# Performance work log

Hardware: AMD Instinct MI355X
Metric: run time of the kernel (lower is better)

## Reference

```python
import jax, jax.numpy as jnp
import numpy as np

MI, DIS, DIN, HID, L, H, NG, H1, OUT = 2048, 1024, 3072, 256, 15, 8, 8, 512, 64
DENOM = 4.0 / 7.0  # (grid_max - grid_min) / (num_grids - 1)
EPS = 1e-5


def _ln(x, g, b):
    m = jnp.mean(x, axis=-1, keepdims=True)
    v = jnp.mean((x - m) ** 2, axis=-1, keepdims=True)
    return (x - m) * jax.lax.rsqrt(v + EPS) * g + b


def _fastkan(x, ln_g, ln_b, grid, Ws, Wb, bb):
    xn = _ln(x, ln_g, ln_b)
    basis = jnp.exp(-(((xn[..., None] - grid) / DENOM) ** 2))  # [N, DIN, NG]
    ret = basis.reshape(x.shape[0], -1) @ Ws.T                  # SplineLinear (no bias)
    return ret + jax.nn.silu(x) @ Wb.T + bb                      # base update


def _hgcn(x, G, W, attn, bias, rW1, rb1, rW2, rb2, ln_g, ln_b, jk_W, jk_b):
    # per-layer multi-head conv: mean_h a_h * G @ (x @ W_h) == G @ (x @ (sum_h a_h W_h / H))
    def step(xc, p):
        W_l, a_l, b_l, rW1_l, rb1_l, rW2_l, rb2_l, g_l, be_l = p
        W_eff = jnp.einsum('h,hio->io', a_l, W_l) / H
        out = G @ (xc @ W_eff) + b_l
        gate = jax.nn.sigmoid(jax.nn.relu(out @ rW1_l.T + rb1_l) @ rW2_l.T + rb2_l)
        out = _ln(out * gate, g_l, be_l)
        out = jnp.where(out >= 0, out, 0.25 * out)  # leaky_relu(0.25); dropout off (eval)
        return out, out
    _, outs = jax.lax.scan(step, x, (W, attn, bias, rW1, rb1, rW2, rb2, ln_g, ln_b))
    jk = jnp.moveaxis(outs, 0, 1).reshape(x.shape[0], L * HID)   # jumping-knowledge concat
    return jk @ jk_W.T + jk_b


def _mlp3(x, W1, b1, W2, b2, W3, b3):
    h = jax.nn.relu(x @ W1.T + b1)
    h = jax.nn.relu(h @ W2.T + b2)
    return jax.nn.relu(h @ W3.T + b3)


def _forward(concat_mi, concat_dis, G_mi, G_dis, AT, A, rbf_grid, mi_kan_ln_g, mi_kan_ln_b, mi_kan_Ws, mi_kan_Wb, mi_kan_bb, dis_kan_ln_g, dis_kan_ln_b, dis_kan_Ws, dis_kan_Wb, dis_kan_bb, mi_W, mi_attn, mi_bias, mi_rW1, mi_rb1, mi_rW2, mi_rb2, mi_ln_g, mi_ln_b, mi_jk_W, mi_jk_b, dis_W, dis_attn, dis_bias, dis_rW1, dis_rb1, dis_rW2, dis_rb2, dis_ln_g, dis_ln_b, dis_jk_W, dis_jk_b, lx_W1, lx_b1, lx_W2, lx_b2, lx_W3, lx_b3, ly_W1, ly_b1, ly_W2, ly_b2, ly_W3, ly_b3, ne_W, ne_b, he_W, he_b, mun_W, mun_b, mue_W, mue_b):
    # AT and A are accepted by the original forward but never used in its body.
    mi_e = _fastkan(concat_mi, mi_kan_ln_g, mi_kan_ln_b, rbf_grid, mi_kan_Ws, mi_kan_Wb, mi_kan_bb)
    dis_e = _fastkan(concat_dis, dis_kan_ln_g, dis_kan_ln_b, rbf_grid, dis_kan_Ws, dis_kan_Wb, dis_kan_bb)
    mi_f = _hgcn(mi_e, G_mi, mi_W, mi_attn, mi_bias, mi_rW1, mi_rb1, mi_rW2, mi_rb2, mi_ln_g, mi_ln_b, mi_jk_W, mi_jk_b)
    dis_f = _hgcn(dis_e, G_dis, dis_W, dis_attn, dis_bias, dis_rW1, dis_rb1, dis_rW2, dis_rb2, dis_ln_g, dis_ln_b, dis_jk_W, dis_jk_b)
    x = _mlp3(mi_f, lx_W1, lx_b1, lx_W2, lx_b2, lx_W3, lx_b3)
    y = _mlp3(dis_f, ly_W1, ly_b1, ly_W2, ly_b2, ly_W3, ly_b3)
    result_h = x @ y.T                                           # [MI, DIS]
    z_node = jax.nn.relu(concat_mi @ ne_W.T + ne_b)              # node_encoders1 (eval: no dropout)
    z_edge = jax.nn.relu(concat_dis @ he_W.T + he_b)             # hyperedge_encoders1
    z_node_mean = z_node @ mun_W.T + mun_b                       # _enc_mu_node (identity act)
    z_edge_mean = z_edge @ mue_W.T + mue_b                       # _enc_mu_hedge
    recon = z_node_mean @ z_edge_mean.T                          # decoder2 with identity act
    score = 0.7 * jax.nn.sigmoid(recon) + 0.3 * jax.nn.sigmoid(result_h)
    return score, recon


def setup_inputs() -> dict:
    ks = iter(jax.random.split(jax.random.key(0), 96))
    nrm = lambda shape, s: jax.random.normal(next(ks), shape, dtype=jnp.float32) * s
    uni = lambda shape: jax.random.uniform(next(ks), shape, dtype=jnp.float32)
    d = {}
    d['concat_mi'] = nrm((MI, DIN), 1.0)
    d['concat_dis'] = nrm((DIS, DIN), 1.0)
    d['G_mi'] = uni((MI, MI)) / MI    # row-normalized dense hypergraph adjacency
    d['G_dis'] = uni((DIS, DIS)) / DIS
    d['AT'] = uni((DIS, MI))
    d['A'] = uni((MI, DIS))
    d['rbf_grid'] = jnp.linspace(-2.0, 2.0, NG).astype(jnp.float32)
    for p in ('mi', 'dis'):
        d[p + '_kan_ln_g'] = jnp.ones((DIN,), jnp.float32)
        d[p + '_kan_ln_b'] = jnp.zeros((DIN,), jnp.float32)
        d[p + '_kan_Ws'] = nrm((HID, DIN * NG), 0.02)
        d[p + '_kan_Wb'] = nrm((HID, DIN), 0.02)
        d[p + '_kan_bb'] = nrm((HID,), 0.01)
        d[p + '_W'] = nrm((L, H, HID, HID), 0.06)
        d[p + '_attn'] = jnp.ones((L, H), jnp.float32)
        d[p + '_bias'] = nrm((L, HID), 0.01)
        d[p + '_rW1'] = nrm((L, HID // 4, HID), 0.05)
        d[p + '_rb1'] = nrm((L, HID // 4), 0.01)
        d[p + '_rW2'] = nrm((L, HID, HID // 4), 0.05)
        d[p + '_rb2'] = nrm((L, HID), 0.01)
        d[p + '_ln_g'] = jnp.ones((L, HID), jnp.float32)
        d[p + '_ln_b'] = jnp.zeros((L, HID), jnp.float32)
        d[p + '_jk_W'] = nrm((HID, L * HID), 0.02)
        d[p + '_jk_b'] = nrm((HID,), 0.01)
    for p in ('lx', 'ly'):
        d[p + '_W1'] = nrm((256, HID), 0.05); d[p + '_b1'] = nrm((256,), 0.01)
        d[p + '_W2'] = nrm((128, 256), 0.05); d[p + '_b2'] = nrm((128,), 0.01)
        d[p + '_W3'] = nrm((64, 128), 0.05); d[p + '_b3'] = nrm((64,), 0.01)
    d['ne_W'] = nrm((H1, DIN), 0.02); d['ne_b'] = nrm((H1,), 0.01)
    d['he_W'] = nrm((H1, DIN), 0.02); d['he_b'] = nrm((H1,), 0.01)
    d['mun_W'] = nrm((OUT, H1), 0.02); d['mun_b'] = nrm((OUT,), 0.01)
    d['mue_W'] = nrm((OUT, H1), 0.02); d['mue_b'] = nrm((OUT,), 0.01)
    return d


def reference(concat_mi, concat_dis, G_mi, G_dis, AT, A, rbf_grid, mi_kan_ln_g, mi_kan_ln_b, mi_kan_Ws, mi_kan_Wb, mi_kan_bb, dis_kan_ln_g, dis_kan_ln_b, dis_kan_Ws, dis_kan_Wb, dis_kan_bb, mi_W, mi_attn, mi_bias, mi_rW1, mi_rb1, mi_rW2, mi_rb2, mi_ln_g, mi_ln_b, mi_jk_W, mi_jk_b, dis_W, dis_attn, dis_bias, dis_rW1, dis_rb1, dis_rW2, dis_rb2, dis_ln_g, dis_ln_b, dis_jk_W, dis_jk_b, lx_W1, lx_b1, lx_W2, lx_b2, lx_W3, lx_b3, ly_W1, ly_b1, ly_W2, ly_b2, ly_W3, ly_b3, ne_W, ne_b, he_W, he_b, mun_W, mun_b, mue_W, mue_b):
    return _forward(concat_mi, concat_dis, G_mi, G_dis, AT, A, rbf_grid, mi_kan_ln_g, mi_kan_ln_b, mi_kan_Ws, mi_kan_Wb, mi_kan_bb, dis_kan_ln_g, dis_kan_ln_b, dis_kan_Ws, dis_kan_Wb, dis_kan_bb, mi_W, mi_attn, mi_bias, mi_rW1, mi_rb1, mi_rW2, mi_rb2, mi_ln_g, mi_ln_b, mi_jk_W, mi_jk_b, dis_W, dis_attn, dis_bias, dis_rW1, dis_rb1, dis_rW2, dis_rb2, dis_ln_g, dis_ln_b, dis_jk_W, dis_jk_b, lx_W1, lx_b1, lx_W2, lx_b2, lx_W3, lx_b3, ly_W1, ly_b1, ly_W2, ly_b2, ly_W3, ly_b3, ne_W, ne_b, he_W, he_b, mun_W, mun_b, mue_W, mue_b)
```

## Files before the change

### kernel.cpp

```cpp
#include <hip/hip_runtime.h>
#include <cstdint>
#include <cstddef>

typedef unsigned short u16;
typedef __attribute__((ext_vector_type(8))) short short8;
typedef __attribute__((ext_vector_type(4))) float f32x4;

#define MI_N  2048
#define DIS_N 1024
#define TOT_N 3072
#define DIN   3072
#define HID   256
#define LL    15
#define NG    8

__device__ __forceinline__ float b2f(u16 u) {
  unsigned int v = ((unsigned int)u) << 16;
  float f;
  __builtin_memcpy(&f, &v, 4);
  return f;
}
__device__ __forceinline__ u16 f2b(float f) {
  unsigned int u;
  __builtin_memcpy(&u, &f, 4);
  u = (u + 0x7fffu + ((u >> 16) & 1u)) >> 16;
  return (u16)u;
}
__device__ __forceinline__ float sigf(float x) { return 1.f / (1.f + __expf(-x)); }

#define NSEG 20
struct CvtJobs {
  const float* src[NSEG];
  u16* dst[NSEG];
  int nblk[NSEG];
  int nseg;
};

__global__ __launch_bounds__(256) void cvt_f2b(CvtJobs j) {
  int b = blockIdx.x, s = 0;
  while (s + 1 < j.nseg && b >= j.nblk[s]) { b -= j.nblk[s]; ++s; }
  const long base = ((long)b * 256 + threadIdx.x) * 8;
  const float4 v0 = *(const float4*)(j.src[s] + base);
  const float4 v1 = *(const float4*)(j.src[s] + base + 4);
  short8 o;
  o[0] = (short)f2b(v0.x); o[1] = (short)f2b(v0.y);
  o[2] = (short)f2b(v0.z); o[3] = (short)f2b(v0.w);
  o[4] = (short)f2b(v1.x); o[5] = (short)f2b(v1.y);
  o[6] = (short)f2b(v1.z); o[7] = (short)f2b(v1.w);
  *(short8*)(j.dst[s] + base) = o;
}

struct GP {
  const u16* A; int lda;
  const u16* B; int ldb;
  void* C; int ldc;
  const float* bias;
  int K;
  int mblk;
};

template <int ACT, int TRANS, int F32OUT, int NCT>
__global__ __launch_bounds__(256) void gemm_bt(GP p0, GP p1) {
  GP p = p0;
  int bx = blockIdx.x;
  if (bx >= p0.mblk) { bx -= p0.mblk; p = p1; }
  const int tid = threadIdx.x;
  const int w = tid >> 6;
  const int lane = tid & 63;
  const int m16 = lane & 15, quad = lane >> 4;
  const int kph = quad * 8;
  const long row0 = (long)bx * 32 + m16;
  const long colBase = (long)blockIdx.y * (16 * NCT);
  f32x4 acc[2][NCT] = {};
  const u16* A0 = p.A + row0 * (long)p.lda + kph;
  const u16* A1 = A0 + 16L * p.lda;
  const u16* Bb = p.B + (colBase + m16) * (long)p.ldb + kph;
  const long bstep = 16L * p.ldb;
  for (int kk = w * 32; kk < p.K; kk += 128) {
    short8 a0 = *(const short8*)(A0 + kk);
    short8 a1 = *(const short8*)(A1 + kk);
#pragma unroll
    for (int c = 0; c < NCT; ++c) {
      short8 b = *(const short8*)(Bb + c * bstep + kk);
      acc[0][c] = __builtin_amdgcn_mfma_f32_16x16x32_bf16(a0, b, acc[0][c], 0, 0, 0);
      acc[1][c] = __builtin_amdgcn_mfma_f32_16x16x32_bf16(a1, b, acc[1][c], 0, 0, 0);
    }
  }
  __shared__ float red[2][64][NCT * 8 + 1];
  float* av = (float*)acc;
  if (w >= 2) {
#pragma unroll
    for (int i = 0; i < NCT * 8; ++i) red[w - 2][lane][i] = av[i];
  }
  __syncthreads();
  if (w < 2) {
#pragma unroll
    for (int i = 0; i < NCT * 8; ++i) av[i] += red[w][lane][i];
  }
  __syncthreads();
  if (w == 1) {
#pragma unroll
    for (int i = 0; i < NCT * 8; ++i) red[0][lane][i] = av[i];
  }
  __syncthreads();
  if (w != 0) return;
#pragma unroll
  for (int i = 0; i < NCT * 8; ++i) av[i] += red[0][lane][i];
#pragma unroll
  for (int c = 0; c < NCT; ++c) {
    const long col = colBase + c * 16 + m16;
    const float bv = p.bias ? p.bias[col] : 0.f;
#pragma unroll
    for (int r = 0; r < 2; ++r) {
      const long orow = (long)bx * 32 + r * 16 + quad * 4;
#pragma unroll
      for (int j = 0; j < 4; ++j) {
        float v = acc[r][c][j] + bv;
        if (ACT == 1) v = fmaxf(v, 0.f);
        if (ACT == 2) v = sigf(v);
        if (F32OUT)
          ((float*)p.C)[(orow + j) * (long)p.ldc + col] = v;
        else if (TRANS)
          ((u16*)p.C)[col * (long)p.ldc + orow + j] = f2b(v);
        else
          ((u16*)p.C)[(orow + j) * (long)p.ldc + col] = f2b(v);
      }
    }
  }
}

struct FKP {
  const u16* xn; const u16* xb;
  const u16* Ws; const u16* Wb;
  float* partial;
  int rowoff;
  int mblk;
};

__global__ __launch_bounds__(256) void fastkan_gemm(FKP p0, FKP p1, const float* grid8) {
  FKP p = p0;
  int bx = blockIdx.x;
  if (bx >= p0.mblk) { bx -= p0.mblk; p = p1; }
  const int chunk = blockIdx.z;
  const int tid = threadIdx.x;
  const int w = tid >> 6;
  const int lane = tid & 63;
  const int m16 = lane & 15, quad = lane >> 4, kph = quad * 8;
  const long row0 = (long)bx * 32 + m16;
  const long colBase = (long)blockIdx.y * 128;
  f32x4 acc[2][8] = {};
  if (chunk < 4) {
    float gv[8];
#pragma unroll
    for (int j = 0; j < 8; ++j) gv[j] = grid8[j];
    const u16* xn0 = p.xn + row0 * (long)DIN;
    const u16* xn1 = xn0 + 16L * DIN;
    const int k0 = chunk * 6144, k1 = k0 + 6144;
    for (int kk = k0 + w * 32; kk < k1; kk += 128) {
      const int d = (kk >> 3) + quad;
      const float x0 = b2f(xn0[d]);
      const float x1 = b2f(xn1[d]);
      short8 a0, a1;
#pragma unroll
      for (int j = 0; j < 8; ++j) {
        float t0 = (x0 - gv[j]) * 1.75f;
        float t1 = (x1 - gv[j]) * 1.75f;
        a0[j] = (short)f2b(__expf(-t0 * t0));
        a1[j] = (short)f2b(__expf(-t1 * t1));
      }
#pragma unroll
      for (int c = 0; c < 8; ++c) {
        const u16* Bp = p.Ws + (colBase + c * 16 + m16) * (long)(DIN * NG) + kk + kph;
        short8 b = *(const short8*)Bp;
        acc[0][c] = __builtin_amdgcn_mfma_f32_16x16x32_bf16(a0, b, acc[0][c], 0, 0, 0);
        acc[1][c] = __builtin_amdgcn_mfma_f32_16x16x32_bf16(a1, b, acc[1][c], 0, 0, 0);
      }
    }
  } else {
    const u16* x0p = p.xb + row0 * (long)DIN + kph;
    const u16* x1p = x0p + 16L * DIN;
    for (int kk = w * 32; kk < DIN; kk += 128) {
      short8 r0 = *(const short8*)(x0p + kk);
      short8 r1 = *(const short8*)(x1p + kk);
      short8 a0, a1;
#pragma unroll
      for (int j = 0; j < 8; ++j) {
        float v0 = b2f((u16)r0[j]);
        float v1 = b2f((u16)r1[j]);
        a0[j] = (short)f2b(v0 * sigf(v0));
        a1[j] = (short)f2b(v1 * sigf(v1));
      }
#pragma unroll
      for (int c = 0; c < 8; ++c) {
        const u16* Bp = p.Wb + (colBase + c * 16 + m16) * (long)DIN + kk + kph;
        short8 b = *(const short8*)Bp;
        acc[0][c] = __builtin_amdgcn_mfma_f32_16x16x32_bf16(a0, b, acc[0][c], 0, 0, 0);
        acc[1][c] = __builtin_amdgcn_mfma_f32_16x16x32_bf16(a1, b, acc[1][c], 0, 0, 0);
      }
    }
  }
  __shared__ float red[2][64][65];
  float* av = (float*)acc;
  if (w >= 2) {
#pragma unroll
    for (int i = 0; i < 64; ++i) red[w - 2][lane][i] = av[i];
  }
  __syncthreads();
  if (w < 2) {
#pragma unroll
    for (int i = 0; i < 64; ++i) av[i] += red[w][lane][i];
  }
  __syncthreads();
  if (w == 1) {
#pragma unroll
    for (int i = 0; i < 64; ++i) red[0][lane][i] = av[i];
  }
  __syncthreads();
  if (w != 0) return;
#pragma unroll
  for (int i = 0; i < 64; ++i) av[i] += red[0][lane][i];
  float* outp = p.partial + ((long)chunk * TOT_N + p.rowoff) * HID;
#pragma unroll
  for (int c = 0; c < 8; ++c) {
    const long col = colBase + c * 16 + m16;
#pragma unroll
    for (int r = 0; r < 2; ++r) {
      const long orow = (long)bx * 32 + r * 16 + quad * 4;
#pragma unroll
      for (int j = 0; j < 4; ++j) outp[(orow + j) * HID + col] = acc[r][c][j];
    }
  }
}

__global__ __launch_bounds__(256) void fk_combine(const float* partial, const float* bb_mi,
                                                  const float* bb_dis, u16* e) {
  const long i = (long)blockIdx.x * 256 + threadIdx.x;
  const int c = (int)(i & 255);
  const long n = i >> 8;
  float s = 0.f;
#pragma unroll
  for (int pI = 0; pI < 5; ++pI) s += partial[(long)pI * TOT_N * HID + i];
  s += (n < MI_N ? bb_mi : bb_dis)[c];
  e[i] = f2b(s);
}

__global__ __launch_bounds__(256) void weff_kernel(const float* Wmi, const float* Ami,
                                                   const float* Wdis, const float* Adis,
                                                   u16* outT) {
  const int b = blockIdx.x;
  const int s = b / 3840;
  const int r = b % 3840;
  const int l = r >> 8;
  const int t = r & 255;
  const int i0 = (t >> 4) << 4;
  const int o0 = (t & 15) << 4;
  const float* W = (s ? Wdis : Wmi) + (long)l * 8 * 65536;
  const float* A = (s ? Adis : Ami) + l * 8;
  const int tx = threadIdx.x & 15;
  const int ty = threadIdx.x >> 4;
  float sum = 0.f;
#pragma unroll
  for (int h = 0; h < 8; ++h)
    sum += A[h] * W[(long)h * 65536 + (long)(i0 + ty) * 256 + o0 + tx];
  sum *= 0.125f;
  __shared__ float tile[16][17];
  tile[ty][tx] = sum;
  __syncthreads();
  outT[((long)s * LL + l) * 65536 + (long)(o0 + ty) * 256 + i0 + tx] = f2b(tile[tx][ty]);
}

__device__ __forceinline__ void breduce2(float& a, float& b) {
  for (int o = 32; o > 0; o >>= 1) {
    a += __shfl_down(a, o);
    b += __shfl_down(b, o);
  }
  __shared__ float sm[8];
  const int w = threadIdx.x >> 6;
  const int lane = threadIdx.x & 63;
  if (lane == 0) { sm[w] = a; sm[4 + w] = b; }
  __syncthreads();
  if (threadIdx.x == 0) {
    sm[0] = sm[0] + sm[1] + sm[2] + sm[3];
    sm[4] = sm[4] + sm[5] + sm[6] + sm[7];
  }
  __syncthreads();
  a = sm[0];
  b = sm[4];
}

__global__ __launch_bounds__(256) void ln_silu(const float* xmi, const float* xdis,
                                               const float* gmi, const float* bmi,
                                               const float* gdis, const float* bdis,
                                               u16* xn, u16* cbf) {
  const int n = blockIdx.x;
  const bool ds = (n >= MI_N);
  const float* x = ds ? xdis + (long)(n - MI_N) * DIN : xmi + (long)n * DIN;
  const float* g = ds ? gdis : gmi;
  const float* be = ds ? bdis : bmi;
  float xv[12];
  float s1 = 0.f, s2 = 0.f;
#pragma unroll
  for (int j = 0; j < 12; ++j) {
    xv[j] = x[j * 256 + threadIdx.x];
    s1 += xv[j];
    s2 += xv[j] * xv[j];
  }
  breduce2(s1, s2);
  const float m = s1 * (1.f / DIN);
  const float inv = rsqrtf(s2 * (1.f / DIN) - m * m + 1e-5f);
#pragma unroll
  for (int j = 0; j < 12; ++j) {
    const int e = j * 256 + threadIdx.x;
    xn[(long)n * DIN + e] = f2b((xv[j] - m) * inv * g[e] + be[e]);
    cbf[(long)n * DIN + e] = f2b(xv[j]);
  }
}

__global__ __launch_bounds__(256) void gate_ln(const u16* hout, const u16* gate,
                                               const float* gmi, const float* bmi,
                                               const float* gdis, const float* bdis,
                                               u16* jk, int l) {
  const int n = blockIdx.x;
  const int c = threadIdx.x;
  const bool ds = (n >= MI_N);
  const float* g = (ds ? gdis : gmi) + l * HID;
  const float* be = (ds ? bdis : bmi) + l * HID;
  const float h = b2f(hout[(long)n * HID + c]) * b2f(gate[(long)n * HID + c]);
  float s1 = h, s2 = h * h;
  breduce2(s1, s2);
  const float m = s1 * (1.f / HID);
  const float var = s2 * (1.f / HID) - m * m;
  float y = (h - m) * rsqrtf(var + 1e-5f) * g[c] + be[c];
  y = (y >= 0.f) ? y : 0.25f * y;
  jk[(long)n * (LL * HID) + l * HID + c] = f2b(y);
}

__global__ __launch_bounds__(256) void final_combine(const float* rh, float* out) {
  const long i = (long)blockIdx.x * 256 + threadIdx.x;
  const float rc = out[(long)MI_N * DIS_N + i];
  out[i] = 0.7f * sigf(rc) + 0.3f * sigf(rh[i]);
}

extern "C" void kernel_launch(void* const* d_in, const int* in_sizes, int n_in,
                              void* d_out, int out_size, void* d_ws, size_t ws_size,
                              hipStream_t stream) {
  const float* concat_mi   = (const float*)d_in[0];
  const float* concat_dis  = (const float*)d_in[1];
  const float* G_mi        = (const float*)d_in[2];
  const float* G_dis       = (const float*)d_in[3];
  const float* rbf_grid    = (const float*)d_in[6];
  const float* mi_kan_ln_g = (const float*)d_in[7];
  const float* mi_kan_ln_b = (const float*)d_in[8];
  const float* mi_kan_Ws   = (const float*)d_in[9];
  const float* mi_kan_Wb   = (const float*)d_in[10];
  const float* mi_kan_bb   = (const float*)d_in[11];
  const float* mi_W        = (const float*)d_in[12];
  const float* mi_attn     = (const float*)d_in[13];
  const float* mi_bias     = (const float*)d_in[14];
  const float* mi_rW1      = (const float*)d_in[15];
  const float* mi_rb1      = (const float*)d_in[16];
  const float* mi_rW2      = (const float*)d_in[17];
  const float* mi_rb2      = (const float*)d_in[18];
  const float* mi_ln_g     = (const float*)d_in[19];
  const float* mi_ln_b     = (const float*)d_in[20];
  const float* mi_jk_W     = (const float*)d_in[21];
  const float* mi_jk_b     = (const float*)d_in[22];
  const float* dis_kan_ln_g = (const float*)d_in[23];
  const float* dis_kan_ln_b = (const float*)d_in[24];
  const float* dis_kan_Ws  = (const float*)d_in[25];
  const float* dis_kan_Wb  = (const float*)d_in[26];
  const float* dis_kan_bb  = (const float*)d_in[27];
  const float* dis_W       = (const float*)d_in[28];
  const float* dis_attn    = (const float*)d_in[29];
  const float* dis_bias    = (const float*)d_in[30];
  const float* dis_rW1     = (const float*)d_in[31];
  const float* dis_rb1     = (const float*)d_in[32];
  const float* dis_rW2     = (const float*)d_in[33];
  const float* dis_rb2     = (const float*)d_in[34];
  const float* dis_ln_g    = (const float*)d_in[35];
  const float* dis_ln_b    = (const float*)d_in[36];
  const float* dis_jk_W    = (const float*)d_in[37];
  const float* dis_jk_b    = (const float*)d_in[38];
  const float* lx_W1 = (const float*)d_in[39]; const float* lx_b1 = (const float*)d_in[40];
  const float* lx_W2 = (const float*)d_in[41]; const float* lx_b2 = (const float*)d_in[42];
  const float* lx_W3 = (const float*)d_in[43]; const float* lx_b3 = (const float*)d_in[44];
  const float* ly_W1 = (const float*)d_in[45]; const float* ly_b1 = (const float*)d_in[46];
  const float* ly_W2 = (const float*)d_in[47]; const float* ly_b2 = (const float*)d_in[48];
  const float* ly_W3 = (const float*)d_in[49]; const float* ly_b3 = (const float*)d_in[50];
  const float* ne_W  = (const float*)d_in[51]; const float* ne_b  = (const float*)d_in[52];
  const float* he_W  = (const float*)d_in[53]; const float* he_b  = (const float*)d_in[54];
  const float* mun_W = (const float*)d_in[55]; const float* mun_b = (const float*)d_in[56];
  const float* mue_W = (const float*)d_in[57]; const float* mue_b = (const float*)d_in[58];

  char* wp = (char*)d_ws;
  size_t off = 0;
  auto alloc = [&](size_t bytes) -> void* {
    void* p = wp + off;
    off += (bytes + 255) & ~(size_t)255;
    return p;
  };
  u16* cbf    = (u16*)alloc((size_t)TOT_N * DIN * 2);
  u16* gmib   = (u16*)alloc((size_t)MI_N * MI_N * 2);
  u16* gdisb  = (u16*)alloc((size_t)DIS_N * DIS_N * 2);
  u16* wsb0   = (u16*)alloc((size_t)256 * 24576 * 2);
  u16* wsb1   = (u16*)alloc((size_t)256 * 24576 * 2);
  u16* wbb0   = (u16*)alloc((size_t)256 * 3072 * 2);
  u16* wbb1   = (u16*)alloc((size_t)256 * 3072 * 2);
  u16* jkwb0  = (u16*)alloc((size_t)256 * 3840 * 2);
  u16* jkwb1  = (u16*)alloc((size_t)256 * 3840 * 2);
  u16* rw1b0  = (u16*)alloc((size_t)LL * 64 * 256 * 2);
  u16* rw1b1  = (u16*)alloc((size_t)LL * 64 * 256 * 2);
  u16* rw2b0  = (u16*)alloc((size_t)LL * 256 * 64 * 2);
  u16* rw2b1  = (u16*)alloc((size_t)LL * 256 * 64 * 2);
  u16* lxw1b  = (u16*)alloc((size_t)256 * 256 * 2);
  u16* lxw2b  = (u16*)alloc((size_t)128 * 256 * 2);
  u16* lxw3b  = (u16*)alloc((size_t)64 * 128 * 2);
  u16* lyw1b  = (u16*)alloc((size_t)256 * 256 * 2);
  u16* lyw2b  = (u16*)alloc((size_t)128 * 256 * 2);
  u16* lyw3b  = (u16*)alloc((size_t)64 * 128 * 2);
  u16* neb    = (u16*)alloc((size_t)512 * 3072 * 2);
  u16* heb    = (u16*)alloc((size_t)512 * 3072 * 2);
  u16* munb   = (u16*)alloc((size_t)64 * 512 * 2);
  u16* mueb   = (u16*)alloc((size_t)64 * 512 * 2);
  u16* wefft  = (u16*)alloc((size_t)2 * LL * 65536 * 2);
  u16* e      = (u16*)alloc((size_t)TOT_N * HID * 2);
  u16* t1t    = (u16*)alloc((size_t)HID * TOT_N * 2);
  u16* hout   = (u16*)alloc((size_t)TOT_N * HID * 2);
  u16* g1b    = (u16*)alloc((size_t)TOT_N * 64 * 2);
  u16* gateb  = (u16*)alloc((size_t)TOT_N * HID * 2);
  u16* jk     = (u16*)alloc((size_t)TOT_N * LL * HID * 2);
  u16* fb     = (u16*)alloc((size_t)TOT_N * HID * 2);
  char* regA  = (char*)alloc(35000000);
  u16* xn     = (u16*)regA;
  float* fkp  = (float*)(regA + 18874624);
  u16* h1b    = (u16*)regA;
  u16* h2b    = (u16*)(regA + 1572864);
  u16* xyb    = (u16*)(regA + 2359296);
  float* rh   = (float*)(regA + 2752512);
  u16* zb     = (u16*)(regA + 11141120);
  u16* zm     = (u16*)(regA + 14286848);
  float* outf = (float*)d_out;
  float* rec  = outf + (size_t)MI_N * DIS_N;
  (void)ws_size; (void)in_sizes; (void)n_in; (void)out_size;

  const dim3 B256(256);

  {
    CvtJobs cj{};
    int ns = 0, total = 0;
    auto push = [&](const float* s, u16* dst, int count) {
      cj.src[ns] = s; cj.dst[ns] = dst; cj.nblk[ns] = count / 2048;
      total += count / 2048; ++ns;
    };
    push(G_mi, gmib, MI_N * MI_N);
    push(G_dis, gdisb, DIS_N * DIS_N);
    push(mi_kan_Ws, wsb0, 256 * 24576);
    push(dis_kan_Ws, wsb1, 256 * 24576);
    push(mi_kan_Wb, wbb0, 256 * 3072);
    push(dis_kan_Wb, wbb1, 256 * 3072);
    push(mi_jk_W, jkwb0, 256 * 3840);
    push(dis_jk_W, jkwb1, 256 * 3840);
    push(mi_rW1, rw1b0, LL * 64 * 256);
    push(dis_rW1, rw1b1, LL * 64 * 256);
    push(mi_rW2, rw2b0, LL * 256 * 64);
    push(dis_rW2, rw2b1, LL * 256 * 64);
    push(lx_W1, lxw1b, 256 * 256);
    push(lx_W2, lxw2b, 128 * 256);
    push(lx_W3, lxw3b, 64 * 128);
    push(ly_W1, lyw1b, 256 * 256);
    push(ly_W2, lyw2b, 128 * 256);
    push(ly_W3, lyw3b, 64 * 128);
    push(ne_W, neb, 512 * 3072);
    push(he_W, heb, 512 * 3072);
    cj.nseg = ns;
    cvt_f2b<<<dim3(total), B256, 0, stream>>>(cj);
    CvtJobs cj2{};
    cj2.src[0] = mun_W; cj2.dst[0] = munb; cj2.nblk[0] = (64 * 512) / 2048;
    cj2.src[1] = mue_W; cj2.dst[1] = mueb; cj2.nblk[1] = (64 * 512) / 2048;
    cj2.nseg = 2;
    cvt_f2b<<<dim3(32), B256, 0, stream>>>(cj2);
  }
  ln_silu<<<dim3(TOT_N), B256, 0, stream>>>(concat_mi, concat_dis, mi_kan_ln_g, mi_kan_ln_b,
                                            dis_kan_ln_g, dis_kan_ln_b, xn, cbf);
  weff_kernel<<<dim3(2 * LL * 256), B256, 0, stream>>>(mi_W, mi_attn, dis_W, dis_attn, wefft);
  {
    FKP f0{xn, cbf, wsb0, wbb0, fkp, 0, 64};
    FKP f1{xn + (size_t)MI_N * DIN, cbf + (size_t)MI_N * DIN, wsb1, wbb1, fkp, MI_N, 32};
    fastkan_gemm<<<dim3(96, 2, 5), B256, 0, stream>>>(f0, f1, rbf_grid);
    fk_combine<<<dim3(TOT_N * HID / 256), B256, 0, stream>>>(fkp, mi_kan_bb, dis_kan_bb, e);
  }
  for (int l = 0; l < LL; ++l) {
    const u16* xc0 = (l == 0) ? e : jk + (size_t)(l - 1) * HID;
    const u16* xc1 = (l == 0) ? e + (size_t)MI_N * HID
                              : jk + (size_t)MI_N * LL * HID + (size_t)(l - 1) * HID;
    const int xlda = (l == 0) ? HID : LL * HID;
    GP a0{xc0, xlda, wefft + (size_t)l * 65536, 256, t1t, MI_N, nullptr, 256, 64};
    GP a1{xc1, xlda, wefft + ((size_t)LL + l) * 65536, 256, t1t + (size_t)HID * MI_N, DIS_N,
          nullptr, 256, 32};
    gemm_bt<0, 1, 0, 4><<<dim3(96, 4), B256, 0, stream>>>(a0, a1);
    GP h0{gmib, MI_N, t1t, MI_N, hout, HID, mi_bias + l * HID, MI_N, 64};
    GP h1{gdisb, DIS_N, t1t + (size_t)HID * MI_N, DIS_N, hout + (size_t)MI_N * HID, HID,
          dis_bias + l * HID, DIS_N, 32};
    gemm_bt<0, 0, 0, 4><<<dim3(96, 4), B256, 0, stream>>>(h0, h1);
    GP g0{hout, HID, rw1b0 + (size_t)l * 64 * HID, HID, g1b, 64, mi_rb1 + l * 64, HID, 64};
    GP g1{hout + (size_t)MI_N * HID, HID, rw1b1 + (size_t)l * 64 * HID, HID,
          g1b + (size_t)MI_N * 64, 64, dis_rb1 + l * 64, HID, 32};
    gemm_bt<1, 0, 0, 4><<<dim3(96, 1), B256, 0, stream>>>(g0, g1);
    GP s0{g1b, 64, rw2b0 + (size_t)l * HID * 64, 64, gateb, HID, mi_rb2 + l * HID, 64, 64};
    GP s1{g1b + (size_t)MI_N * 64, 64, rw2b1 + (size_t)l * HID * 64, 64,
          gateb + (size_t)MI_N * HID, HID, dis_rb2 + l * HID, 64, 32};
    gemm_bt<2, 0, 0, 4><<<dim3(96, 4), B256, 0, stream>>>(s0, s1);
    gate_ln<<<dim3(TOT_N), B256, 0, stream>>>(hout, gateb, mi_ln_g, mi_ln_b, dis_ln_g,
                                              dis_ln_b, jk, l);
  }
  {
    GP j0{jk, LL * HID, jkwb0, LL * HID, fb, HID, mi_jk_b, LL * HID, 64};
    GP j1{jk + (size_t)MI_N * LL * HID, LL * HID, jkwb1, LL * HID, fb + (size_t)MI_N * HID,
          HID, dis_jk_b, LL * HID, 32};
    gemm_bt<0, 0, 0, 4><<<dim3(96, 4), B256, 0, stream>>>(j0, j1);
  }
  {
    GP m0{fb, HID, lxw1b, HID, h1b, 256, lx_b1, HID, 64};
    GP m1{fb + (size_t)MI_N * HID, HID, lyw1b, HID, h1b + (size_t)MI_N * 256, 256, ly_b1,
          HID, 32};
    gemm_bt<1, 0, 0, 4><<<dim3(96, 4), B256, 0, stream>>>(m0, m1);
    GP n0{h1b, 256, lxw2b, 256, h2b, 128, lx_b2, 256, 64};
    GP n1{h1b + (size_t)MI_N * 256, 256, lyw2b, 256, h2b + (size_t)MI_N * 128, 128, ly_b2,
          256, 32};
    gemm_bt<1, 0, 0, 4><<<dim3(96, 2), B256, 0, stream>>>(n0, n1);
    GP o0{h2b, 128, lxw3b, 128, xyb, 64, lx_b3, 128, 64};
    GP o1{h2b + (size_t)MI_N * 128, 128, lyw3b, 128, xyb + (size_t)MI_N * 64, 64, ly_b3,
          128, 32};
    gemm_bt<1, 0, 0, 4><<<dim3(96, 1), B256, 0, stream>>>(o0, o1);
  }
  {
    GP r0{xyb, 64, xyb + (size_t)MI_N * 64, 64, rh, DIS_N, nullptr, 64, 64};
    gemm_bt<0, 0, 1, 4><<<dim3(64, 16), B256, 0, stream>>>(r0, r0);
  }
  {
    GP e0{cbf, DIN, neb, DIN, zb, 512, ne_b, DIN, 64};
    GP e1{cbf + (size_t)MI_N * DIN, DIN, heb, DIN, zb + (size_t)MI_N * 512, 512, he_b, DIN,
          32};
    gemm_bt<1, 0, 0, 4><<<dim3(96, 8), B256, 0, stream>>>(e0, e1);
  }
  {
    GP u0{zb, 512, munb, 512, zm, 64, mun_b, 512, 64};
    GP u1{zb + (size_t)MI_N * 512, 512, mueb, 512, zm + (size_t)MI_N * 64, 64, mue_b, 512,
          32};
    gemm_bt<0, 0, 0, 4><<<dim3(96, 1), B256, 0, stream>>>(u0, u1);
  }
  {
    GP c0{zm, 64, zm + (size_t)MI_N * 64, 64, rec, DIS_N, nullptr, 64, 64};
    gemm_bt<0, 0, 1, 4><<<dim3(64, 16), B256, 0, stream>>>(c0, c0);
  }
  final_combine<<<dim3(MI_N * DIS_N / 256), B256, 0, stream>>>(rh, outf);
}
```

Baseline: 1.458 ms.

## Retile FastKAN GEMM to full-width 16-row tiles with deeper split-K

The FastKAN spline/base GEMM now gives each block 16 rows and all 256 output columns, instead of 32 rows by 128 columns. Split-K grows from 5 to 9 chunks, and the combine kernel and partial buffer are enlarged to match. Each Gaussian RBF basis value is now computed once per row rather than once per column block, and per-thread x values are prefetched into registers. Pairs of floats are packed to bf16 with v_cvt_pk_bf16_f32. The trade-off is that each weight load now feeds one MFMA instead of two, so weight traffic through L2 roughly doubles, and the larger split-K means more partial-sum writes and reads.

```diff
diff --git a/kernel.cpp b/kernel.cpp
--- a/kernel.cpp
+++ b/kernel.cpp
@@ -27,6 +27,11 @@
   return (u16)u;
 }
 __device__ __forceinline__ float sigf(float x) { return 1.f / (1.f + __expf(-x)); }
+__device__ __forceinline__ unsigned cvtpk(float a, float b) {
+  unsigned r;
+  asm("v_cvt_pk_bf16_f32 %0, %1, %2" : "=v"(r) : "v"(a), "v"(b));
+  return r;
+}
 
 #define NSEG 20
 struct CvtJobs {
@@ -146,56 +151,52 @@
   const int w = tid >> 6;
   const int lane = tid & 63;
   const int m16 = lane & 15, quad = lane >> 4, kph = quad * 8;
-  const long row0 = (long)bx * 32 + m16;
-  const long colBase = (long)blockIdx.y * 128;
-  f32x4 acc[2][8] = {};
-  if (chunk < 4) {
+  const long row0 = (long)bx * 16 + m16;
+  f32x4 acc[16] = {};
+  if (chunk < 8) {
     float gv[8];
 #pragma unroll
     for (int j = 0; j < 8; ++j) gv[j] = grid8[j];
     const u16* xn0 = p.xn + row0 * (long)DIN;
-    const u16* xn1 = xn0 + 16L * DIN;
-    const int k0 = chunk * 6144, k1 = k0 + 6144;
-    for (int kk = k0 + w * 32; kk < k1; kk += 128) {
-      const int d = (kk >> 3) + quad;
-      const float x0 = b2f(xn0[d]);
-      const float x1 = b2f(xn1[d]);
-      short8 a0, a1;
-#pragma unroll
-      for (int j = 0; j < 8; ++j) {
-        float t0 = (x0 - gv[j]) * 1.75f;
-        float t1 = (x1 - gv[j]) * 1.75f;
-        a0[j] = (short)f2b(__expf(-t0 * t0));
-        a1[j] = (short)f2b(__expf(-t1 * t1));
+    const int d0 = chunk * 384 + w * 4 + quad;
+    u16 xr[24];
+#pragma unroll
+    for (int t = 0; t < 24; ++t) xr[t] = xn0[d0 + 16 * t];
+    const u16* Bb = p.Ws + (long)m16 * (DIN * NG) + chunk * 3072 + w * 32 + kph;
+#pragma unroll 2
+    for (int t = 0; t < 24; ++t) {
+      const float x0 = b2f(xr[t]);
+      union { short8 s; unsigned u[4]; } a0;
+#pragma unroll
+      for (int jj = 0; jj < 4; ++jj) {
+        float da = x0 - gv[2 * jj];
+        float db = x0 - gv[2 * jj + 1];
+        a0.u[jj] = cvtpk(__expf(da * da * -3.0625f), __expf(db * db * -3.0625f));
       }
 #pragma unroll
-      for (int c = 0; c < 8; ++c) {
-        const u16* Bp = p.Ws + (colBase + c * 16 + m16) * (long)(DIN * NG) + kk + kph;
-        short8 b = *(const short8*)Bp;
-        acc[0][c] = __builtin_amdgcn_mfma_f32_16x16x32_bf16(a0, b, acc[0][c], 0, 0, 0);
-        acc[1][c] = __builtin_amdgcn_mfma_f32_16x16x32_bf16(a1, b, acc[1][c], 0, 0, 0);
+      for (int c = 0; c < 16; ++c) {
+        short8 b = *(const short8*)(Bb + (long)c * (16 * DIN * NG) + t * 128);
+        acc[c] = __builtin_amdgcn_mfma_f32_16x16x32_bf16(a0.s, b, acc[c], 0, 0, 0);
       }
     }
   } else {
     const u16* x0p = p.xb + row0 * (long)DIN + kph;
-    const u16* x1p = x0p + 16L * DIN;
-    for (int kk = w * 32; kk < DIN; kk += 128) {
+    const u16* Bb = p.Wb + (long)m16 * DIN + w * 32 + kph;
+#pragma unroll 2
+    for (int t = 0; t < 24; ++t) {
+      const int kk = w * 32 + t * 128;
       short8 r0 = *(const short8*)(x0p + kk);
-      short8 r1 = *(const short8*)(x1p + kk);
-      short8 a0, a1;
-#pragma unroll
-      for (int j = 0; j < 8; ++j) {
-        float v0 = b2f((u16)r0[j]);
-        float v1 = b2f((u16)r1[j]);
-        a0[j] = (short)f2b(v0 * sigf(v0));
-        a1[j] = (short)f2b(v1 * sigf(v1));
+      union { short8 s; unsigned u[4]; } a0;
+#pragma unroll
+      for (int jj = 0; jj < 4; ++jj) {
+        float va = b2f((u16)r0[2 * jj]);
+        float vb = b2f((u16)r0[2 * jj + 1]);
+        a0.u[jj] = cvtpk(va * sigf(va), vb * sigf(vb));
       }
 #pragma unroll
-      for (int c = 0; c < 8; ++c) {
-        const u16* Bp = p.Wb + (colBase + c * 16 + m16) * (long)DIN + kk + kph;
-        short8 b = *(const short8*)Bp;
-        acc[0][c] = __builtin_amdgcn_mfma_f32_16x16x32_bf16(a0, b, acc[0][c], 0, 0, 0);
-        acc[1][c] = __builtin_amdgcn_mfma_f32_16x16x32_bf16(a1, b, acc[1][c], 0, 0, 0);
+      for (int c = 0; c < 16; ++c) {
+        short8 b = *(const short8*)(Bb + (long)c * (16 * DIN) + t * 128);
+        acc[c] = __builtin_amdgcn_mfma_f32_16x16x32_bf16(a0.s, b, acc[c], 0, 0, 0);
       }
     }
   }
@@ -221,14 +222,11 @@
   for (int i = 0; i < 64; ++i) av[i] += red[0][lane][i];
   float* outp = p.partial + ((long)chunk * TOT_N + p.rowoff) * HID;
 #pragma unroll
-  for (int c = 0; c < 8; ++c) {
-    const long col = colBase + c * 16 + m16;
-#pragma unroll
-    for (int r = 0; r < 2; ++r) {
-      const long orow = (long)bx * 32 + r * 16 + quad * 4;
-#pragma unroll
-      for (int j = 0; j < 4; ++j) outp[(orow + j) * HID + col] = acc[r][c][j];
-    }
+  for (int c = 0; c < 16; ++c) {
+    const long col = c * 16 + m16;
+    const long orow = (long)bx * 16 + quad * 4;
+#pragma unroll
+    for (int j = 0; j < 4; ++j) outp[(orow + j) * HID + col] = acc[c][j];
   }
 }
 
@@ -239,7 +237,7 @@
   const long n = i >> 8;
   float s = 0.f;
 #pragma unroll
-  for (int pI = 0; pI < 5; ++pI) s += partial[(long)pI * TOT_N * HID + i];
+  for (int pI = 0; pI < 9; ++pI) s += partial[(long)pI * TOT_N * HID + i];
   s += (n < MI_N ? bb_mi : bb_dis)[c];
   e[i] = f2b(s);
 }
@@ -430,7 +428,7 @@
   u16* gateb  = (u16*)alloc((size_t)TOT_N * HID * 2);
   u16* jk     = (u16*)alloc((size_t)TOT_N * LL * HID * 2);
   u16* fb     = (u16*)alloc((size_t)TOT_N * HID * 2);
-  char* regA  = (char*)alloc(35000000);
+  char* regA  = (char*)alloc(47300000);
   u16* xn     = (u16*)regA;
   float* fkp  = (float*)(regA + 18874624);
   u16* h1b    = (u16*)regA;
@@ -484,9 +482,9 @@
                                             dis_kan_ln_g, dis_kan_ln_b, xn, cbf);
   weff_kernel<<<dim3(2 * LL * 256), B256, 0, stream>>>(mi_W, mi_attn, dis_W, dis_attn, wefft);
   {
-    FKP f0{xn, cbf, wsb0, wbb0, fkp, 0, 64};
-    FKP f1{xn + (size_t)MI_N * DIN, cbf + (size_t)MI_N * DIN, wsb1, wbb1, fkp, MI_N, 32};
-    fastkan_gemm<<<dim3(96, 2, 5), B256, 0, stream>>>(f0, f1, rbf_grid);
+    FKP f0{xn, cbf, wsb0, wbb0, fkp, 0, 128};
+    FKP f1{xn + (size_t)MI_N * DIN, cbf + (size_t)MI_N * DIN, wsb1, wbb1, fkp, MI_N, 64};
+    fastkan_gemm<<<dim3(192, 1, 9), B256, 0, stream>>>(f0, f1, rbf_grid);
     fk_combine<<<dim3(TOT_N * HID / 256), B256, 0, stream>>>(fkp, mi_kan_bb, dis_kan_bb, e);
   }
   for (int l = 0; l < LL; ++l) {
```

Result: slower. 1.601 ms (+9.8%).

## Fuse per-layer HGCN chain into one kernel with next-layer projection

Applied to the files above, without the earlier changes.

Each layer's propagation GEMM, both gate GEMMs, the sigmoid gate, the layernorm with leaky ReLU, and the next layer's x@W_eff projection now run in a single kernel. Intermediates stay in shared memory, and the transposed projection is ping-ponged between two buffers. This cuts five launches per layer down to one and removes the global round trips for hout, g1 and the gate. In exchange only 96 blocks run, each with a full-K G-row GEMM that has no LDS staging of operands, so parallelism and memory efficiency per layer may drop.

```diff
diff --git a/kernel.cpp b/kernel.cpp
--- a/kernel.cpp
+++ b/kernel.cpp
@@ -244,6 +244,159 @@
   e[i] = f2b(s);
 }
 
+struct HLP {
+  const u16* G; const u16* t1t; u16* t1t_next; const u16* weff_next;
+  const float* bias; const u16* rw1; const float* rb1;
+  const u16* rw2; const float* rb2; const float* lng; const float* lnb;
+  u16* jk; int M; int mblk;
+};
+
+__global__ __launch_bounds__(256) void hgcn_layer(HLP p0, HLP p1) {
+  HLP p = p0;
+  int bx = blockIdx.x;
+  if (bx >= p0.mblk) { bx -= p0.mblk; p = p1; }
+  const int tid = threadIdx.x;
+  const int w = tid >> 6, lane = tid & 63;
+  const int m16 = lane & 15, quad = lane >> 4, kph = quad * 8;
+  const int cb = w * 64;
+  const long row0 = (long)bx * 32;
+  __shared__ __align__(16) u16 hl[32][264];
+  __shared__ __align__(16) u16 gl[32][264];
+  __shared__ __align__(16) u16 g1l[32][72];
+
+  {
+    f32x4 acc[2][4] = {};
+    const u16* A0 = p.G + (row0 + m16) * (long)p.M + kph;
+    const u16* A1 = A0 + 16L * p.M;
+    const u16* Bb = p.t1t + (long)(cb + m16) * p.M + kph;
+    const long bstep = 16L * p.M;
+    for (int kk = 0; kk < p.M; kk += 32) {
+      short8 a0 = *(const short8*)(A0 + kk);
+      short8 a1 = *(const short8*)(A1 + kk);
+#pragma unroll
+      for (int c = 0; c < 4; ++c) {
+        short8 b = *(const short8*)(Bb + c * bstep + kk);
+        acc[0][c] = __builtin_amdgcn_mfma_f32_16x16x32_bf16(a0, b, acc[0][c], 0, 0, 0);
+        acc[1][c] = __builtin_amdgcn_mfma_f32_16x16x32_bf16(a1, b, acc[1][c], 0, 0, 0);
+      }
+    }
+#pragma unroll
+    for (int c = 0; c < 4; ++c) {
+      const int col = cb + c * 16 + m16;
+      const float bv = p.bias[col];
+#pragma unroll
+      for (int r = 0; r < 2; ++r) {
+        const int orow = r * 16 + quad * 4;
+#pragma unroll
+        for (int j = 0; j < 4; ++j) hl[orow + j][col] = f2b(acc[r][c][j] + bv);
+      }
+    }
+  }
+  __syncthreads();
+  {
+    f32x4 acc[2] = {};
+    const u16* Bb = p.rw1 + (long)(w * 16 + m16) * 256 + kph;
+#pragma unroll
+    for (int kk = 0; kk < 256; kk += 32) {
+      short8 a0 = *(const short8*)&hl[m16][kk + kph];
+      short8 a1 = *(const short8*)&hl[16 + m16][kk + kph];
+      short8 b = *(const short8*)(Bb + kk);
+      acc[0] = __builtin_amdgcn_mfma_f32_16x16x32_bf16(a0, b, acc[0], 0, 0, 0);
+      acc[1] = __builtin_amdgcn_mfma_f32_16x16x32_bf16(a1, b, acc[1], 0, 0, 0);
+    }
+    const int col = w * 16 + m16;
+    const float bv = p.rb1[col];
+#pragma unroll
+    for (int r = 0; r < 2; ++r) {
+      const int orow = r * 16 + quad * 4;
+#pragma unroll
+      for (int j = 0; j < 4; ++j) g1l[orow + j][col] = f2b(fmaxf(acc[r][j] + bv, 0.f));
+    }
+  }
+  __syncthreads();
+  {
+    f32x4 acc[2][4] = {};
+    const u16* Bb = p.rw2 + (long)(cb + m16) * 64 + kph;
+#pragma unroll
+    for (int kk = 0; kk < 64; kk += 32) {
+      short8 a0 = *(const short8*)&g1l[m16][kk + kph];
+      short8 a1 = *(const short8*)&g1l[16 + m16][kk + kph];
+#pragma unroll
+      for (int c = 0; c < 4; ++c) {
+        short8 b = *(const short8*)(Bb + c * (16L * 64) + kk);
+        acc[0][c] = __builtin_amdgcn_mfma_f32_16x16x32_bf16(a0, b, acc[0][c], 0, 0, 0);
+        acc[1][c] = __builtin_amdgcn_mfma_f32_16x16x32_bf16(a1, b, acc[1][c], 0, 0, 0);
+      }
+    }
+#pragma unroll
+    for (int c = 0; c < 4; ++c) {
+      const int col = cb + c * 16 + m16;
+      const float bv = p.rb2[col];
+#pragma unroll
+      for (int r = 0; r < 2; ++r) {
+        const int orow = r * 16 + quad * 4;
+#pragma unroll
+        for (int j = 0; j < 4; ++j) gl[orow + j][col] = f2b(sigf(acc[r][c][j] + bv));
+      }
+    }
+  }
+  __syncthreads();
+  {
+    const int row = tid >> 3;
+    const int sub = tid & 7;
+    float pv[32];
+    float s1 = 0.f, s2 = 0.f;
+#pragma unroll
+    for (int i = 0; i < 32; ++i) {
+      const int col = sub * 32 + i;
+      const float v = b2f(hl[row][col]) * b2f(gl[row][col]);
+      pv[i] = v; s1 += v; s2 += v * v;
+    }
+#pragma unroll
+    for (int o = 1; o < 8; o <<= 1) { s1 += __shfl_xor(s1, o); s2 += __shfl_xor(s2, o); }
+    const float m = s1 * (1.f / HID);
+    const float inv = rsqrtf(s2 * (1.f / HID) - m * m + 1e-5f);
+    u16* jrow = p.jk + (row0 + row) * (long)(LL * HID);
+#pragma unroll
+    for (int i = 0; i < 32; ++i) {
+      const int col = sub * 32 + i;
+      float y = (pv[i] - m) * inv * p.lng[col] + p.lnb[col];
+      y = (y >= 0.f) ? y : 0.25f * y;
+      const u16 yb = f2b(y);
+      jrow[col] = yb;
+      gl[row][col] = yb;
+    }
+  }
+  if (!p.weff_next) return;
+  __syncthreads();
+  {
+    f32x4 acc[2][4] = {};
+    const u16* Bb = p.weff_next + (long)(cb + m16) * 256 + kph;
+#pragma unroll
+    for (int kk = 0; kk < 256; kk += 32) {
+      short8 a0 = *(const short8*)&gl[m16][kk + kph];
+      short8 a1 = *(const short8*)&gl[16 + m16][kk + kph];
+#pragma unroll
+      for (int c = 0; c < 4; ++c) {
+        short8 b = *(const short8*)(Bb + c * (16L * 256) + kk);
+        acc[0][c] = __builtin_amdgcn_mfma_f32_16x16x32_bf16(a0, b, acc[0][c], 0, 0, 0);
+        acc[1][c] = __builtin_amdgcn_mfma_f32_16x16x32_bf16(a1, b, acc[1][c], 0, 0, 0);
+      }
+    }
+#pragma unroll
+    for (int c = 0; c < 4; ++c) {
+      const long col = cb + c * 16 + m16;
+#pragma unroll
+      for (int r = 0; r < 2; ++r) {
+        const int orow = r * 16 + quad * 4;
+#pragma unroll
+        for (int j = 0; j < 4; ++j)
+          p.t1t_next[col * (long)p.M + row0 + orow + j] = f2b(acc[r][c][j]);
+      }
+    }
+  }
+}
+
 __global__ __launch_bounds__(256) void weff_kernel(const float* Wmi, const float* Ami,
                                                    const float* Wdis, const float* Adis,
                                                    u16* outT) {
@@ -314,25 +467,6 @@
     xn[(long)n * DIN + e] = f2b((xv[j] - m) * inv * g[e] + be[e]);
     cbf[(long)n * DIN + e] = f2b(xv[j]);
   }
-}
-
-__global__ __launch_bounds__(256) void gate_ln(const u16* hout, const u16* gate,
-                                               const float* gmi, const float* bmi,
-                                               const float* gdis, const float* bdis,
-                                               u16* jk, int l) {
-  const int n = blockIdx.x;
-  const int c = threadIdx.x;
-  const bool ds = (n >= MI_N);
-  const float* g = (ds ? gdis : gmi) + l * HID;
-  const float* be = (ds ? bdis : bmi) + l * HID;
-  const float h = b2f(hout[(long)n * HID + c]) * b2f(gate[(long)n * HID + c]);
-  float s1 = h, s2 = h * h;
-  breduce2(s1, s2);
-  const float m = s1 * (1.f / HID);
-  const float var = s2 * (1.f / HID) - m * m;
-  float y = (h - m) * rsqrtf(var + 1e-5f) * g[c] + be[c];
-  y = (y >= 0.f) ? y : 0.25f * y;
-  jk[(long)n * (LL * HID) + l * HID + c] = f2b(y);
 }
 
 __global__ __launch_bounds__(256) void final_combine(const float* rh, float* out) {
@@ -425,9 +559,7 @@
   u16* wefft  = (u16*)alloc((size_t)2 * LL * 65536 * 2);
   u16* e      = (u16*)alloc((size_t)TOT_N * HID * 2);
   u16* t1t    = (u16*)alloc((size_t)HID * TOT_N * 2);
-  u16* hout   = (u16*)alloc((size_t)TOT_N * HID * 2);
-  u16* g1b    = (u16*)alloc((size_t)TOT_N * 64 * 2);
-  u16* gateb  = (u16*)alloc((size_t)TOT_N * HID * 2);
+  u16* t1t2   = (u16*)alloc((size_t)HID * TOT_N * 2);
   u16* jk     = (u16*)alloc((size_t)TOT_N * LL * HID * 2);
   u16* fb     = (u16*)alloc((size_t)TOT_N * HID * 2);
   char* regA  = (char*)alloc(35000000);
@@ -489,29 +621,30 @@
     fastkan_gemm<<<dim3(96, 2, 5), B256, 0, stream>>>(f0, f1, rbf_grid);
     fk_combine<<<dim3(TOT_N * HID / 256), B256, 0, stream>>>(fkp, mi_kan_bb, dis_kan_bb, e);
   }
-  for (int l = 0; l < LL; ++l) {
-    const u16* xc0 = (l == 0) ? e : jk + (size_t)(l - 1) * HID;
-    const u16* xc1 = (l == 0) ? e + (size_t)MI_N * HID
-                              : jk + (size_t)MI_N * LL * HID + (size_t)(l - 1) * HID;
-    const int xlda = (l == 0) ? HID : LL * HID;
-    GP a0{xc0, xlda, wefft + (size_t)l * 65536, 256, t1t, MI_N, nullptr, 256, 64};
-    GP a1{xc1, xlda, wefft + ((size_t)LL + l) * 65536, 256, t1t + (size_t)HID * MI_N, DIS_N,
-          nullptr, 256, 32};
+  {
+    GP a0{e, HID, wefft, 256, t1t, MI_N, nullptr, 256, 64};
+    GP a1{e + (size_t)MI_N * HID, HID, wefft + (size_t)LL * 65536, 256,
+          t1t + (size_t)HID * MI_N, DIS_N, nullptr, 256, 32};
     gemm_bt<0, 1, 0, 4><<<dim3(96, 4), B256, 0, stream>>>(a0, a1);
-    GP h0{gmib, MI_N, t1t, MI_N, hout, HID, mi_bias + l * HID, MI_N, 64};
-    GP h1{gdisb, DIS_N, t1t + (size_t)HID * MI_N, DIS_N, hout + (size_t)MI_N * HID, HID,
-          dis_bias + l * HID, DIS_N, 32};
-    gemm_bt<0, 0, 0, 4><<<dim3(96, 4), B256, 0, stream>>>(h0, h1);
-    GP g0{hout, HID, rw1b0 + (size_t)l * 64 * HID, HID, g1b, 64, mi_rb1 + l * 64, HID, 64};
-    GP g1{hout + (size_t)MI_N * HID, HID, rw1b1 + (size_t)l * 64 * HID, HID,
-          g1b + (size_t)MI_N * 64, 64, dis_rb1 + l * 64, HID, 32};
-    gemm_bt<1, 0, 0, 4><<<dim3(96, 1), B256, 0, stream>>>(g0, g1);
-    GP s0{g1b, 64, rw2b0 + (size_t)l * HID * 64, 64, gateb, HID, mi_rb2 + l * HID, 64, 64};
-    GP s1{g1b + (size_t)MI_N * 64, 64, rw2b1 + (size_t)l * HID * 64, 64,
-          gateb + (size_t)MI_N * HID, HID, dis_rb2 + l * HID, 64, 32};
-    gemm_bt<2, 0, 0, 4><<<dim3(96, 4), B256, 0, stream>>>(s0, s1);
-    gate_ln<<<dim3(TOT_N), B256, 0, stream>>>(hout, gateb, mi_ln_g, mi_ln_b, dis_ln_g,
-                                              dis_ln_b, jk, l);
+  }
+  {
+    u16* tc = t1t;
+    u16* tn = t1t2;
+    for (int l = 0; l < LL; ++l) {
+      const bool last = (l == LL - 1);
+      HLP h0{gmib, tc, tn, last ? nullptr : wefft + (size_t)(l + 1) * 65536,
+             mi_bias + l * HID, rw1b0 + (size_t)l * 64 * HID, mi_rb1 + l * 64,
+             rw2b0 + (size_t)l * HID * 64, mi_rb2 + l * HID,
+             mi_ln_g + l * HID, mi_ln_b + l * HID, jk + (size_t)l * HID, MI_N, 64};
+      HLP h1{gdisb, tc + (size_t)HID * MI_N, tn + (size_t)HID * MI_N,
+             last ? nullptr : wefft + ((size_t)LL + l + 1) * 65536,
+             dis_bias + l * HID, rw1b1 + (size_t)l * 64 * HID, dis_rb1 + l * 64,
+             rw2b1 + (size_t)l * HID * 64, dis_rb2 + l * HID,
+             dis_ln_g + l * HID, dis_ln_b + l * HID,
+             jk + (size_t)MI_N * LL * HID + (size_t)l * HID, DIS_N, 32};
+      hgcn_layer<<<dim3(96), B256, 0, stream>>>(h0, h1);
+      u16* t = tc; tc = tn; tn = t;
+    }
   }
   {
     GP j0{jk, LL * HID, jkwb0, LL * HID, fb, HID, mi_jk_b, LL * HID, 64};
```

New measurement: 1.613 ms. 10.6% more time.
